# Kernel optimization log

Hardware: AMD Instinct MI355X
Metric: run time of the kernel (lower is better)

The kernel has to match this reference:

```python
import jax, jax.numpy as jnp
import numpy as np

B = 64          # decode batch (one token per sequence)
HID = 4096      # hidden_size
HQ = 32         # num query heads
HKV = 8         # num kv heads (GQA, groups = 4)
D = 128         # head_dim
BS = 16         # block_size of paged KV cache
MAXB = 64       # max blocks per sequence -> max context 1024
MAXPOS = 4096   # rope table length
TOTAL_SLOTS = B * MAXB * BS


def setup_inputs() -> dict:
    key = jax.random.key(0)
    ks = jax.random.split(key, 10)
    hidden = jax.random.normal(ks[0], (B, 1, HID), jnp.float32)
    context_lens = jax.random.randint(ks[1], (B,), 512, BS * MAXB + 1).astype(jnp.int32)
    positions = (context_lens - 1).reshape(B, 1)  # decoding token position
    # each sequence owns a contiguous range of blocks
    block_tables = jnp.arange(B * MAXB, dtype=jnp.int32).reshape(B, MAXB)
    last = context_lens - 1
    slot_mapping = (block_tables[jnp.arange(B), last // BS] * BS + last % BS).astype(jnp.int32)
    inv_freq = 1.0 / (10000.0 ** (jnp.arange(0, D, 2, dtype=jnp.float32) / D))
    freqs = jnp.outer(jnp.arange(MAXPOS, dtype=jnp.float32), inv_freq)  # [MAXPOS, D/2]
    cos, sin = jnp.cos(freqs), jnp.sin(freqs)
    key_cache = jax.random.normal(ks[2], (TOTAL_SLOTS, HKV, D), jnp.float32) * 0.5
    value_cache = jax.random.normal(ks[3], (TOTAL_SLOTS, HKV, D), jnp.float32) * 0.5
    Wq = jax.random.normal(ks[4], (HQ * D, HID), jnp.float32) * 0.02
    Wk = jax.random.normal(ks[5], (HKV * D, HID), jnp.float32) * 0.02
    Wv = jax.random.normal(ks[6], (HKV * D, HID), jnp.float32) * 0.02
    Wo = jax.random.normal(ks[7], (HID, HQ * D), jnp.float32) * 0.02
    return dict(hidden=hidden, positions=positions, cos=cos, sin=sin,
                key_cache=key_cache, value_cache=value_cache,
                slot_mapping=slot_mapping, block_tables=block_tables,
                context_lens=context_lens, Wq=Wq, Wk=Wk, Wv=Wv, Wo=Wo)


def reference(hidden, positions, cos, sin, key_cache, value_cache,
              slot_mapping, block_tables, context_lens, Wq, Wk, Wv, Wo):
    b, s, _ = hidden.shape  # s == 1 (paged decode path)
    q = (hidden @ Wq.T).reshape(b, s, HQ, D)
    k = (hidden @ Wk.T).reshape(b, s, HKV, D)
    v = (hidden @ Wv.T).reshape(b, s, HKV, D)
    # rotary embedding (half-split convention)
    c = cos[positions][:, :, None, :]  # [b,s,1,D/2]
    sn = sin[positions][:, :, None, :]
    def rope(x):
        x1, x2 = jnp.split(x, 2, axis=-1)
        return jnp.concatenate([x1 * c - x2 * sn, x2 * c + x1 * sn], axis=-1)
    q, k = rope(q), rope(k)
    # scatter current token's K/V into the paged cache via slot_mapping
    kc = key_cache.at[slot_mapping].set(k.reshape(-1, HKV, D))
    vc = value_cache.at[slot_mapping].set(v.reshape(-1, HKV, D))
    # gather each sequence's KV via block tables
    T = MAXB * BS
    t = jnp.arange(T)
    slots = block_tables[:, t // BS] * BS + (t % BS)  # [b, T]
    keys = kc[slots]   # [b, T, HKV, D]
    vals = vc[slots]   # [b, T, HKV, D]
    # GQA attention, q has one token per sequence
    G = HQ // HKV
    qg = q.reshape(b, HKV, G, D)
    scores = jnp.einsum('bkgd,btkd->bkgt', qg, keys) / jnp.sqrt(jnp.float32(D))
    mask = t[None, :] < context_lens[:, None]  # [b, T]
    scores = jnp.where(mask[:, None, None, :], scores, -jnp.inf)
    p = jax.nn.softmax(scores, axis=-1)
    out = jnp.einsum('bkgt,btkd->bkgd', p, vals).reshape(b, 1, HQ * D)
    return out @ Wo.T
```

## Files before the change

### kernel.cpp

```cpp
#include <hip/hip_runtime.h>

#define B_    64
#define HID_  4096
#define HQ_   32
#define HKV_  8
#define D_    128
#define BS_   16
#define MAXB_ 64

#define KS1     32
#define KCHUNK  (HID_ / KS1)
#define NSTEP   (KCHUNK / 32)
#define QKV_ROWS 6144
#define O_ROWS   4096
#define SPLITS  8

#define REGION_SZ ((size_t)KS1 * QKV_ROWS * 64)
#define QKVF_SZ  ((size_t)64 * 6144)
#define XB_SZ    ((size_t)HID_ * 64)

typedef __attribute__((ext_vector_type(8))) short bf16x8;
typedef __attribute__((ext_vector_type(4))) float f32x4;

__device__ inline unsigned short f2bf(float x) {
  union { float f; unsigned u; } v; v.f = x;
  unsigned r = v.u + 0x7fff + ((v.u >> 16) & 1);
  return (unsigned short)(r >> 16);
}
__device__ inline float bf2f(unsigned short h) {
  union { float f; unsigned u; } v; v.u = ((unsigned)h) << 16; return v.f;
}

__global__ __launch_bounds__(256) void convert_x(
    const float* __restrict__ X, unsigned short* __restrict__ XBhi,
    unsigned short* __restrict__ XBlo)
{
  int idx = blockIdx.x * 256 + threadIdx.x;
  int kg = idx >> 6, b = idx & 63;
  const float* xp = X + (size_t)b * HID_ + kg * 8;
  float4 a = *(const float4*)xp, c = *(const float4*)(xp + 4);
  float xs[8] = {a.x, a.y, a.z, a.w, c.x, c.y, c.z, c.w};
  unsigned short hi[8], lo[8];
  #pragma unroll
  for (int j = 0; j < 8; ++j) {
    hi[j] = f2bf(xs[j]);
    lo[j] = f2bf(xs[j] - bf2f(hi[j]));
  }
  *(uint4*)(XBhi + (size_t)idx * 8) = *(const uint4*)hi;
  *(uint4*)(XBlo + (size_t)idx * 8) = *(const uint4*)lo;
}

__global__ __launch_bounds__(256, 4) void gemm_mfma(
    const float* __restrict__ W0, const float* __restrict__ W1,
    const float* __restrict__ W2,
    const unsigned short* __restrict__ XBhi,
    const unsigned short* __restrict__ XBlo,
    int split1, int split2, int rows_total, float* __restrict__ part)
{
  const int tid = threadIdx.x;
  const int l   = tid & 63;
  const int w   = tid >> 6;
  const int r0  = blockIdx.x * 128 + w * 32;
  const int k0  = blockIdx.y * KCHUNK;

  const float* W; int rloc;
  if (r0 < split1)      { W = W0; rloc = r0; }
  else if (r0 < split2) { W = W1; rloc = r0 - split1; }
  else                  { W = W2; rloc = r0 - split2; }

  const int lm = l & 15;
  const int lk = l >> 4;

  const float* wp0 = W + (size_t)(rloc + lm) * HID_ + k0 + lk * 8;
  const float* wp1 = wp0 + (size_t)16 * HID_;
  const unsigned short* bh = XBhi + ((size_t)(k0 / 8 + lk) * 64 + lm) * 8;
  const unsigned short* bl = XBlo + ((size_t)(k0 / 8 + lk) * 64 + lm) * 8;

  f32x4 acc[2][4];
  #pragma unroll
  for (int rt = 0; rt < 2; ++rt)
    #pragma unroll
    for (int ct = 0; ct < 4; ++ct)
      #pragma unroll
      for (int i = 0; i < 4; ++i) acc[rt][ct][i] = 0.f;

  #pragma unroll
  for (int ks = 0; ks < NSTEP; ++ks) {
    bf16x8 Bh[4], Bl[4];
    #pragma unroll
    for (int ct = 0; ct < 4; ++ct) {
      Bh[ct] = *(const bf16x8*)(bh + (size_t)ks * 2048 + ct * 128);
      Bl[ct] = *(const bf16x8*)(bl + (size_t)ks * 2048 + ct * 128);
    }
    #pragma unroll
    for (int rt = 0; rt < 2; ++rt) {
      const float* wp = (rt ? wp1 : wp0) + ks * 32;
      float4 a0 = *(const float4*)wp;
      float4 a1 = *(const float4*)(wp + 4);
      float xs[8] = {a0.x, a0.y, a0.z, a0.w, a1.x, a1.y, a1.z, a1.w};
      bf16x8 Ah, Al;
      #pragma unroll
      for (int j = 0; j < 8; ++j) {
        unsigned short h = f2bf(xs[j]);
        Ah[j] = (short)h;
        Al[j] = (short)f2bf(xs[j] - bf2f(h));
      }
      #pragma unroll
      for (int ct = 0; ct < 4; ++ct) {
        acc[rt][ct] = __builtin_amdgcn_mfma_f32_16x16x32_bf16(Ah, Bh[ct], acc[rt][ct], 0, 0, 0);
        acc[rt][ct] = __builtin_amdgcn_mfma_f32_16x16x32_bf16(Al, Bh[ct], acc[rt][ct], 0, 0, 0);
        acc[rt][ct] = __builtin_amdgcn_mfma_f32_16x16x32_bf16(Ah, Bl[ct], acc[rt][ct], 0, 0, 0);
      }
    }
  }

  #pragma unroll
  for (int rt = 0; rt < 2; ++rt)
    #pragma unroll
    for (int ct = 0; ct < 4; ++ct) {
      int row = r0 + rt * 16 + lk * 4;
      int bat = ct * 16 + lm;
      #pragma unroll
      for (int i = 0; i < 4; ++i)
        part[((size_t)blockIdx.y * rows_total + row + i) * 64 + bat] = acc[rt][ct][i];
    }
}

__global__ __launch_bounds__(256) void reduce_rope(
    const float* __restrict__ part, const float* __restrict__ cosT,
    const float* __restrict__ sinT, const int* __restrict__ positions,
    float* __restrict__ qkvf)
{
  const int bb  = threadIdx.x & 63;
  const int cid = blockIdx.x * 4 + (threadIdx.x >> 6);
  const int pos = positions[bb];

  if (cid < 2048) {
    const int hq = cid >> 6, d0 = cid & 63;
    const int r1 = hq * 128 + d0;
    float x1 = 0.f, x2 = 0.f;
    #pragma unroll 8
    for (int ks = 0; ks < KS1; ++ks) {
      x1 += part[((size_t)ks * QKV_ROWS + r1) * 64 + bb];
      x2 += part[((size_t)ks * QKV_ROWS + r1 + 64) * 64 + bb];
    }
    float c = cosT[pos * 64 + d0], s = sinT[pos * 64 + d0];
    const float scale = 0.08838834764831843f;
    qkvf[(size_t)(bb * 32 + hq) * 128 + d0]      = (x1 * c - x2 * s) * scale;
    qkvf[(size_t)(bb * 32 + hq) * 128 + d0 + 64] = (x2 * c + x1 * s) * scale;
  } else if (cid < 2560) {
    const int c2 = cid - 2048;
    const int kh = c2 >> 6, d0 = c2 & 63;
    const int r1 = 4096 + kh * 128 + d0;
    float x1 = 0.f, x2 = 0.f;
    #pragma unroll 8
    for (int ks = 0; ks < KS1; ++ks) {
      x1 += part[((size_t)ks * QKV_ROWS + r1) * 64 + bb];
      x2 += part[((size_t)ks * QKV_ROWS + r1 + 64) * 64 + bb];
    }
    float c = cosT[pos * 64 + d0], s = sinT[pos * 64 + d0];
    qkvf[262144 + (size_t)(bb * 8 + kh) * 128 + d0]      = x1 * c - x2 * s;
    qkvf[262144 + (size_t)(bb * 8 + kh) * 128 + d0 + 64] = x2 * c + x1 * s;
  } else {
    const int c2 = cid - 2560;
    const int kh = c2 >> 6, d0 = c2 & 63;
    const int r1 = 5120 + kh * 128 + d0;
    float x1 = 0.f, x2 = 0.f;
    #pragma unroll 8
    for (int ks = 0; ks < KS1; ++ks) {
      x1 += part[((size_t)ks * QKV_ROWS + r1) * 64 + bb];
      x2 += part[((size_t)ks * QKV_ROWS + r1 + 64) * 64 + bb];
    }
    qkvf[327680 + (size_t)(bb * 8 + kh) * 128 + d0]      = x1;
    qkvf[327680 + (size_t)(bb * 8 + kh) * 128 + d0 + 64] = x2;
  }
}

__global__ __launch_bounds__(256, 8) void attn_split(
    const float* __restrict__ qkvf, const float* __restrict__ kcache,
    const float* __restrict__ vcache, const int* __restrict__ btab,
    const int* __restrict__ ctxlen,
    float* __restrict__ part_o,
    float* __restrict__ part_ml)
{
  const int bid = blockIdx.x;
  const int s   = bid & (SPLITS - 1);
  const int bh  = bid >> 3;
  const int b = bh >> 3, h = bh & 7;
  const int ctx   = ctxlen[b];
  const int chunk = (ctx + SPLITS - 1) / SPLITS;
  const int t0 = s * chunk;
  const int t1 = min(ctx, t0 + chunk);
  const int n  = t1 - t0;
  const int last = ctx - 1;

  const int tid  = threadIdx.x;
  const int half = tid >> 5;
  const int d4   = tid & 31;

  __shared__ float sc[4][128];
  __shared__ float wred[4][4][128];
  __shared__ float red[4][2];

  float4 qf[4];
  #pragma unroll
  for (int g = 0; g < 4; ++g)
    qf[g] = *(const float4*)(qkvf + (size_t)(b * 32 + h * 4 + g) * 128 + d4 * 4);

  const float* knew = qkvf + 262144 + (size_t)(b * 8 + h) * 128;
  const float* vnew = qkvf + 327680 + (size_t)(b * 8 + h) * 128;

  for (int t = t0 + half; t < t1; t += 8) {
    const float* kp;
    if (t == last) kp = knew;
    else {
      int slot = btab[b * MAXB_ + (t >> 4)] * BS_ + (t & 15);
      kp = kcache + ((size_t)slot * HKV_ + h) * D_;
    }
    float4 kv = *(const float4*)(kp + d4 * 4);
    float p0 = qf[0].x * kv.x + qf[0].y * kv.y + qf[0].z * kv.z + qf[0].w * kv.w;
    float p1 = qf[1].x * kv.x + qf[1].y * kv.y + qf[1].z * kv.z + qf[1].w * kv.w;
    float p2 = qf[2].x * kv.x + qf[2].y * kv.y + qf[2].z * kv.z + qf[2].w * kv.w;
    float p3 = qf[3].x * kv.x + qf[3].y * kv.y + qf[3].z * kv.z + qf[3].w * kv.w;
    #pragma unroll
    for (int m = 16; m >= 1; m >>= 1) {
      p0 += __shfl_xor(p0, m);
      p1 += __shfl_xor(p1, m);
      p2 += __shfl_xor(p2, m);
      p3 += __shfl_xor(p3, m);
    }
    if (d4 == 0) {
      int i = t - t0;
      sc[0][i] = p0; sc[1][i] = p1; sc[2][i] = p2; sc[3][i] = p3;
    }
  }
  __syncthreads();

  {
    const int w = tid >> 6, l = tid & 63;
    float mx = -1e30f;
    for (int i = l; i < n; i += 64) mx = fmaxf(mx, sc[w][i]);
    #pragma unroll
    for (int m = 32; m >= 1; m >>= 1) mx = fmaxf(mx, __shfl_xor(mx, m));
    float lsum = 0.f;
    for (int i = l; i < n; i += 64) {
      float p = __expf(sc[w][i] - mx);
      sc[w][i] = p;
      lsum += p;
    }
    #pragma unroll
    for (int m = 32; m >= 1; m >>= 1) lsum += __shfl_xor(lsum, m);
    if (l == 0) { red[w][0] = mx; red[w][1] = lsum; }
  }
  __syncthreads();

  float acc[4][4] = {{0.f}};
  for (int t = t0 + half; t < t1; t += 8) {
    const float* vp;
    if (t == last) vp = vnew;
    else {
      int slot = btab[b * MAXB_ + (t >> 4)] * BS_ + (t & 15);
      vp = vcache + ((size_t)slot * HKV_ + h) * D_;
    }
    float4 vv = *(const float4*)(vp + d4 * 4);
    int i = t - t0;
    #pragma unroll
    for (int g = 0; g < 4; ++g) {
      float p = sc[g][i];
      acc[g][0] += p * vv.x; acc[g][1] += p * vv.y;
      acc[g][2] += p * vv.z; acc[g][3] += p * vv.w;
    }
  }
  #pragma unroll
  for (int g = 0; g < 4; ++g)
    #pragma unroll
    for (int j = 0; j < 4; ++j)
      acc[g][j] += __shfl_xor(acc[g][j], 32);
  if ((tid & 32) == 0) {
    int wv = tid >> 6;
    #pragma unroll
    for (int g = 0; g < 4; ++g)
      #pragma unroll
      for (int j = 0; j < 4; ++j)
        wred[wv][g][d4 * 4 + j] = acc[g][j];
  }
  __syncthreads();

  for (int idx = tid; idx < 512; idx += 256) {
    int g = idx >> 7, d = idx & 127;
    float v = wred[0][g][d] + wred[1][g][d] + wred[2][g][d] + wred[3][g][d];
    part_o[(size_t)bid * 512 + idx] = v;
  }
  if (tid < 8) part_ml[(size_t)bid * 8 + tid] = red[tid >> 1][tid & 1];
}

__global__ __launch_bounds__(256) void attn_combine_xb(
    const float* __restrict__ part_o, const float* __restrict__ part_ml,
    unsigned short* __restrict__ XBhi, unsigned short* __restrict__ XBlo)
{
  const int bh = blockIdx.x;
  const int b = bh >> 3, h = bh & 7;
  const int tid = threadIdx.x;

  __shared__ float Sg[SPLITS][4];
  __shared__ float Dg[4];

  if (tid < 32) {
    int s = tid >> 2, g = tid & 3;
    float m = part_ml[((size_t)bh * SPLITS + s) * 8 + g * 2];
    float l = part_ml[((size_t)bh * SPLITS + s) * 8 + g * 2 + 1];
    float M = m;
    #pragma unroll
    for (int k = 4; k <= 16; k <<= 1) M = fmaxf(M, __shfl_xor(M, k));
    float scl = __expf(m - M);
    float dl = l * scl;
    #pragma unroll
    for (int k = 4; k <= 16; k <<= 1) dl += __shfl_xor(dl, k);
    Sg[s][g] = scl;
    if (s == 0) Dg[g] = dl;
  }
  __syncthreads();

  for (int idx = tid; idx < 512; idx += 256) {
    int g = idx >> 7, d = idx & 127;
    float num = 0.f;
    #pragma unroll
    for (int s = 0; s < SPLITS; ++s)
      num += Sg[s][g] * part_o[((size_t)bh * SPLITS + s) * 512 + idx];
    float val = num / Dg[g];
    int col = (h * 4 + g) * 128 + d;
    int kg = col >> 3, j = col & 7;
    unsigned short hi = f2bf(val);
    unsigned short lo = f2bf(val - bf2f(hi));
    XBhi[((size_t)kg * 64 + b) * 8 + j] = hi;
    XBlo[((size_t)kg * 64 + b) * 8 + j] = lo;
  }
}

__global__ __launch_bounds__(256) void reduce_out_t(
    const float* __restrict__ part, float* __restrict__ out)
{
  __shared__ float t[64][65];
  const int i0 = blockIdx.x * 64;
  const int lane = threadIdx.x & 63, q = threadIdx.x >> 6;

  #pragma unroll
  for (int rr = q; rr < 64; rr += 4) {
    float s = 0.f;
    #pragma unroll 8
    for (int ks = 0; ks < KS1; ++ks)
      s += part[((size_t)ks * O_ROWS + i0 + rr) * 64 + lane];
    t[rr][lane] = s;
  }
  __syncthreads();
  #pragma unroll
  for (int rr = q; rr < 64; rr += 4)
    out[(size_t)rr * O_ROWS + i0 + lane] = t[lane][rr];
}

extern "C" void kernel_launch(void* const* d_in, const int* in_sizes, int n_in,
                              void* d_out, int out_size, void* d_ws, size_t ws_size,
                              hipStream_t stream)
{
  (void)in_sizes; (void)n_in; (void)out_size; (void)ws_size;
  const float* hidden    = (const float*)d_in[0];
  const int*   positions = (const int*)d_in[1];
  const float* cosT      = (const float*)d_in[2];
  const float* sinT      = (const float*)d_in[3];
  const float* kcache    = (const float*)d_in[4];
  const float* vcache    = (const float*)d_in[5];
  const int*   btab      = (const int*)d_in[7];
  const int*   ctx       = (const int*)d_in[8];
  const float* Wq        = (const float*)d_in[9];
  const float* Wk        = (const float*)d_in[10];
  const float* Wv        = (const float*)d_in[11];
  const float* Wo        = (const float*)d_in[12];
  float* out = (float*)d_out;

  float* ws      = (float*)d_ws;
  float* region  = ws;
  float* qkvf    = region + REGION_SZ;
  unsigned short* XBhi = (unsigned short*)(qkvf + QKVF_SZ);
  unsigned short* XBlo = XBhi + XB_SZ;
  float* part1   = region;
  float* part_o  = region;
  float* part_ml = region + (size_t)B_ * HKV_ * SPLITS * 512;
  float* part3   = region;

  convert_x<<<128, 256, 0, stream>>>(hidden, XBhi, XBlo);
  gemm_mfma<<<dim3(QKV_ROWS / 128, KS1), 256, 0, stream>>>(
      Wq, Wk, Wv, XBhi, XBlo, 4096, 5120, QKV_ROWS, part1);
  reduce_rope<<<768, 256, 0, stream>>>(part1, cosT, sinT, positions, qkvf);
  attn_split<<<B_ * HKV_ * SPLITS, 256, 0, stream>>>(
      qkvf, kcache, vcache, btab, ctx, part_o, part_ml);
  attn_combine_xb<<<B_ * HKV_, 256, 0, stream>>>(part_o, part_ml, XBhi, XBlo);
  gemm_mfma<<<dim3(O_ROWS / 128, KS1), 256, 0, stream>>>(
      Wo, Wo, Wo, XBhi, XBlo, O_ROWS, O_ROWS, O_ROWS, part3);
  reduce_out_t<<<O_ROWS / 64, 256, 0, stream>>>(part3, out);
}
```

Baseline: 224.1 us.

## Stage weight tiles through LDS with async double-buffered global_load_lds

The GEMM kernel now streams fp32 weight tiles into double-buffered shared memory using direct global-to-LDS loads with an XOR swizzle. The next k-step's load is issued while the current one is computed, instead of each wave loading its own rows straight from global memory. The QKV projection also drops its split-K factor from 32 to 16, which halves the partial-sum traffic, with kchunk and nstep passed at runtime. The costs are lower occupancy (launch bounds go from 4 to 3), a barrier every k-step, and fewer blocks in the QKV GEMM.

```diff
diff --git a/kernel.cpp b/kernel.cpp
--- a/kernel.cpp
+++ b/kernel.cpp
@@ -8,14 +8,13 @@
 #define BS_   16
 #define MAXB_ 64
 
-#define KS1     32
-#define KCHUNK  (HID_ / KS1)
-#define NSTEP   (KCHUNK / 32)
+#define KSQ     16
+#define KSO     32
 #define QKV_ROWS 6144
 #define O_ROWS   4096
 #define SPLITS  8
 
-#define REGION_SZ ((size_t)KS1 * QKV_ROWS * 64)
+#define REGION_SZ ((size_t)KSO * O_ROWS * 64)
 #define QKVF_SZ  ((size_t)64 * 6144)
 #define XB_SZ    ((size_t)HID_ * 64)
 
@@ -50,18 +49,21 @@
   *(uint4*)(XBlo + (size_t)idx * 8) = *(const uint4*)lo;
 }
 
-__global__ __launch_bounds__(256, 4) void gemm_mfma(
+__global__ __launch_bounds__(256, 3) void gemm_mfma(
     const float* __restrict__ W0, const float* __restrict__ W1,
     const float* __restrict__ W2,
     const unsigned short* __restrict__ XBhi,
     const unsigned short* __restrict__ XBlo,
-    int split1, int split2, int rows_total, float* __restrict__ part)
-{
+    int split1, int split2, int rows_total, int kchunk, int nstep,
+    float* __restrict__ part)
+{
+  __shared__ float Abuf[2][128 * 32];
+
   const int tid = threadIdx.x;
   const int l   = tid & 63;
   const int w   = tid >> 6;
-  const int r0  = blockIdx.x * 128 + w * 32;
-  const int k0  = blockIdx.y * KCHUNK;
+  const int r0  = blockIdx.x * 128;
+  const int k0  = blockIdx.y * kchunk;
 
   const float* W; int rloc;
   if (r0 < split1)      { W = W0; rloc = r0; }
@@ -71,10 +73,28 @@
   const int lm = l & 15;
   const int lk = l >> 4;
 
-  const float* wp0 = W + (size_t)(rloc + lm) * HID_ + k0 + lk * 8;
-  const float* wp1 = wp0 + (size_t)16 * HID_;
+  const float* Wb = W + (size_t)rloc * HID_ + k0;
   const unsigned short* bh = XBhi + ((size_t)(k0 / 8 + lk) * 64 + lm) * 8;
   const unsigned short* bl = XBlo + ((size_t)(k0 / 8 + lk) * 64 + lm) * 8;
+
+  const int sidx0 = tid;
+  const int wbase = tid & ~63;
+
+  #define ISSUE(buf, step)                                                   \
+    {                                                                        \
+      const float* Wk = Wb + (size_t)(step) * 32;                            \
+      _Pragma("unroll")                                                      \
+      for (int c = 0; c < 4; ++c) {                                          \
+        int idx = c * 256 + sidx0;                                           \
+        int row = idx >> 3, cg = idx & 7;                                    \
+        int g = cg ^ (row & 7);                                              \
+        const float* gsrc = Wk + (size_t)row * HID_ + g * 4;                 \
+        float* ldst = &Abuf[buf][(size_t)(c * 256 + wbase) * 4];             \
+        __builtin_amdgcn_global_load_lds(                                    \
+            (const __attribute__((address_space(1))) unsigned int*)gsrc,     \
+            (__attribute__((address_space(3))) unsigned int*)ldst, 16, 0, 0);\
+      }                                                                      \
+    }
 
   f32x4 acc[2][4];
   #pragma unroll
@@ -84,19 +104,28 @@
       #pragma unroll
       for (int i = 0; i < 4; ++i) acc[rt][ct][i] = 0.f;
 
-  #pragma unroll
-  for (int ks = 0; ks < NSTEP; ++ks) {
+  ISSUE(0, 0);
+
+  for (int s = 0; s < nstep; ++s) {
+    __syncthreads();
+    if (s + 1 < nstep) ISSUE((s + 1) & 1, s + 1);
+
     bf16x8 Bh[4], Bl[4];
     #pragma unroll
     for (int ct = 0; ct < 4; ++ct) {
-      Bh[ct] = *(const bf16x8*)(bh + (size_t)ks * 2048 + ct * 128);
-      Bl[ct] = *(const bf16x8*)(bl + (size_t)ks * 2048 + ct * 128);
-    }
+      Bh[ct] = *(const bf16x8*)(bh + (size_t)s * 2048 + ct * 128);
+      Bl[ct] = *(const bf16x8*)(bl + (size_t)s * 2048 + ct * 128);
+    }
+
+    const float* A = Abuf[s & 1];
     #pragma unroll
     for (int rt = 0; rt < 2; ++rt) {
-      const float* wp = (rt ? wp1 : wp0) + ks * 32;
-      float4 a0 = *(const float4*)wp;
-      float4 a1 = *(const float4*)(wp + 4);
+      int r = w * 32 + rt * 16 + lm;
+      const float* base = A + r * 32;
+      int g0 = (2 * lk) ^ (r & 7);
+      int g1 = (2 * lk + 1) ^ (r & 7);
+      float4 a0 = *(const float4*)(base + g0 * 4);
+      float4 a1 = *(const float4*)(base + g1 * 4);
       float xs[8] = {a0.x, a0.y, a0.z, a0.w, a1.x, a1.y, a1.z, a1.w};
       bf16x8 Ah, Al;
       #pragma unroll
@@ -113,12 +142,13 @@
       }
     }
   }
+  #undef ISSUE
 
   #pragma unroll
   for (int rt = 0; rt < 2; ++rt)
     #pragma unroll
     for (int ct = 0; ct < 4; ++ct) {
-      int row = r0 + rt * 16 + lk * 4;
+      int row = r0 + w * 32 + rt * 16 + lk * 4;
       int bat = ct * 16 + lm;
       #pragma unroll
       for (int i = 0; i < 4; ++i)
@@ -140,7 +170,7 @@
     const int r1 = hq * 128 + d0;
     float x1 = 0.f, x2 = 0.f;
     #pragma unroll 8
-    for (int ks = 0; ks < KS1; ++ks) {
+    for (int ks = 0; ks < KSQ; ++ks) {
       x1 += part[((size_t)ks * QKV_ROWS + r1) * 64 + bb];
       x2 += part[((size_t)ks * QKV_ROWS + r1 + 64) * 64 + bb];
     }
@@ -154,7 +184,7 @@
     const int r1 = 4096 + kh * 128 + d0;
     float x1 = 0.f, x2 = 0.f;
     #pragma unroll 8
-    for (int ks = 0; ks < KS1; ++ks) {
+    for (int ks = 0; ks < KSQ; ++ks) {
       x1 += part[((size_t)ks * QKV_ROWS + r1) * 64 + bb];
       x2 += part[((size_t)ks * QKV_ROWS + r1 + 64) * 64 + bb];
     }
@@ -167,7 +197,7 @@
     const int r1 = 5120 + kh * 128 + d0;
     float x1 = 0.f, x2 = 0.f;
     #pragma unroll 8
-    for (int ks = 0; ks < KS1; ++ks) {
+    for (int ks = 0; ks < KSQ; ++ks) {
       x1 += part[((size_t)ks * QKV_ROWS + r1) * 64 + bb];
       x2 += part[((size_t)ks * QKV_ROWS + r1 + 64) * 64 + bb];
     }
@@ -348,7 +378,7 @@
   for (int rr = q; rr < 64; rr += 4) {
     float s = 0.f;
     #pragma unroll 8
-    for (int ks = 0; ks < KS1; ++ks)
+    for (int ks = 0; ks < KSO; ++ks)
       s += part[((size_t)ks * O_ROWS + i0 + rr) * 64 + lane];
     t[rr][lane] = s;
   }
@@ -388,13 +418,13 @@
   float* part3   = region;
 
   convert_x<<<128, 256, 0, stream>>>(hidden, XBhi, XBlo);
-  gemm_mfma<<<dim3(QKV_ROWS / 128, KS1), 256, 0, stream>>>(
-      Wq, Wk, Wv, XBhi, XBlo, 4096, 5120, QKV_ROWS, part1);
+  gemm_mfma<<<dim3(QKV_ROWS / 128, KSQ), 256, 0, stream>>>(
+      Wq, Wk, Wv, XBhi, XBlo, 4096, 5120, QKV_ROWS, HID_ / KSQ, HID_ / KSQ / 32, part1);
   reduce_rope<<<768, 256, 0, stream>>>(part1, cosT, sinT, positions, qkvf);
   attn_split<<<B_ * HKV_ * SPLITS, 256, 0, stream>>>(
       qkvf, kcache, vcache, btab, ctx, part_o, part_ml);
   attn_combine_xb<<<B_ * HKV_, 256, 0, stream>>>(part_o, part_ml, XBhi, XBlo);
-  gemm_mfma<<<dim3(O_ROWS / 128, KS1), 256, 0, stream>>>(
-      Wo, Wo, Wo, XBhi, XBlo, O_ROWS, O_ROWS, O_ROWS, part3);
+  gemm_mfma<<<dim3(O_ROWS / 128, KSO), 256, 0, stream>>>(
+      Wo, Wo, Wo, XBhi, XBlo, O_ROWS, O_ROWS, O_ROWS, HID_ / KSO, HID_ / KSO / 32, part3);
   reduce_out_t<<<O_ROWS / 64, 256, 0, stream>>>(part3, out);
 }
```

After: 213.2 us. 4.9% less time.

## Fuse attention into a single-pass online softmax and halve GEMM split-K

Applied to the files above, without the earlier changes.

The attention split kernel now reads K and V in the same loop and keeps a per-thread online softmax state (running max, sum and accumulator). Per-half and per-wave states are merged at the end, so the shared-memory score buffer and two of the barriers go away. Block-table entries are staged in shared memory, and the new token's K/V is handled outside the main loop instead of being branched on every iteration. Separately, the GEMM split-K factor drops from 32 to 16, with partial unrolling and a lower occupancy hint. This halves the partial-sum traffic in the reduce kernels but gives the GEMMs fewer blocks and longer per-block loops.

```diff
diff --git a/kernel.cpp b/kernel.cpp
--- a/kernel.cpp
+++ b/kernel.cpp
@@ -8,14 +8,13 @@
 #define BS_   16
 #define MAXB_ 64
 
-#define KS1     32
-#define KCHUNK  (HID_ / KS1)
-#define NSTEP   (KCHUNK / 32)
+#define KS      16
+#define KCHUNK  (HID_ / KS)
 #define QKV_ROWS 6144
 #define O_ROWS   4096
 #define SPLITS  8
 
-#define REGION_SZ ((size_t)KS1 * QKV_ROWS * 64)
+#define REGION_SZ ((size_t)KS * QKV_ROWS * 64)
 #define QKVF_SZ  ((size_t)64 * 6144)
 #define XB_SZ    ((size_t)HID_ * 64)
 
@@ -84,8 +83,8 @@
       #pragma unroll
       for (int i = 0; i < 4; ++i) acc[rt][ct][i] = 0.f;
 
-  #pragma unroll
-  for (int ks = 0; ks < NSTEP; ++ks) {
+  #pragma unroll 2
+  for (int ks = 0; ks < KCHUNK / 32; ++ks) {
     bf16x8 Bh[4], Bl[4];
     #pragma unroll
     for (int ct = 0; ct < 4; ++ct) {
@@ -140,7 +139,7 @@
     const int r1 = hq * 128 + d0;
     float x1 = 0.f, x2 = 0.f;
     #pragma unroll 8
-    for (int ks = 0; ks < KS1; ++ks) {
+    for (int ks = 0; ks < KS; ++ks) {
       x1 += part[((size_t)ks * QKV_ROWS + r1) * 64 + bb];
       x2 += part[((size_t)ks * QKV_ROWS + r1 + 64) * 64 + bb];
     }
@@ -154,7 +153,7 @@
     const int r1 = 4096 + kh * 128 + d0;
     float x1 = 0.f, x2 = 0.f;
     #pragma unroll 8
-    for (int ks = 0; ks < KS1; ++ks) {
+    for (int ks = 0; ks < KS; ++ks) {
       x1 += part[((size_t)ks * QKV_ROWS + r1) * 64 + bb];
       x2 += part[((size_t)ks * QKV_ROWS + r1 + 64) * 64 + bb];
     }
@@ -167,7 +166,7 @@
     const int r1 = 5120 + kh * 128 + d0;
     float x1 = 0.f, x2 = 0.f;
     #pragma unroll 8
-    for (int ks = 0; ks < KS1; ++ks) {
+    for (int ks = 0; ks < KS; ++ks) {
       x1 += part[((size_t)ks * QKV_ROWS + r1) * 64 + bb];
       x2 += part[((size_t)ks * QKV_ROWS + r1 + 64) * 64 + bb];
     }
@@ -176,7 +175,7 @@
   }
 }
 
-__global__ __launch_bounds__(256, 8) void attn_split(
+__global__ __launch_bounds__(256, 4) void attn_split(
     const float* __restrict__ qkvf, const float* __restrict__ kcache,
     const float* __restrict__ vcache, const int* __restrict__ btab,
     const int* __restrict__ ctxlen,
@@ -191,107 +190,144 @@
   const int chunk = (ctx + SPLITS - 1) / SPLITS;
   const int t0 = s * chunk;
   const int t1 = min(ctx, t0 + chunk);
-  const int n  = t1 - t0;
   const int last = ctx - 1;
+  const int tEnd = min(t1, last);
 
   const int tid  = threadIdx.x;
   const int half = tid >> 5;
   const int d4   = tid & 31;
 
-  __shared__ float sc[4][128];
-  __shared__ float wred[4][4][128];
-  __shared__ float red[4][2];
+  __shared__ int   sblk[16];
+  __shared__ float wm[4][4], wl[4][4];
+  __shared__ float wacc[4][4][128];
+
+  const int blk0 = t0 >> 4;
+  if (tid < 16) {
+    int ib = blk0 + tid;
+    sblk[tid] = (ib < MAXB_) ? btab[b * MAXB_ + ib] : 0;
+  }
+  __syncthreads();
 
   float4 qf[4];
   #pragma unroll
   for (int g = 0; g < 4; ++g)
     qf[g] = *(const float4*)(qkvf + (size_t)(b * 32 + h * 4 + g) * 128 + d4 * 4);
 
-  const float* knew = qkvf + 262144 + (size_t)(b * 8 + h) * 128;
-  const float* vnew = qkvf + 327680 + (size_t)(b * 8 + h) * 128;
-
-  for (int t = t0 + half; t < t1; t += 8) {
-    const float* kp;
-    if (t == last) kp = knew;
-    else {
-      int slot = btab[b * MAXB_ + (t >> 4)] * BS_ + (t & 15);
-      kp = kcache + ((size_t)slot * HKV_ + h) * D_;
-    }
-    float4 kv = *(const float4*)(kp + d4 * 4);
+  float m[4], l[4], acc[4][4];
+  #pragma unroll
+  for (int g = 0; g < 4; ++g) {
+    m[g] = -1e30f; l[g] = 0.f;
+    #pragma unroll
+    for (int j = 0; j < 4; ++j) acc[g][j] = 0.f;
+  }
+
+  for (int t = t0 + half; t < tEnd; t += 8) {
+    int slot = sblk[(t >> 4) - blk0] * BS_ + (t & 15);
+    const float* base = kcache + ((size_t)slot * HKV_ + h) * D_ + d4 * 4;
+    const float* vbas = vcache + ((size_t)slot * HKV_ + h) * D_ + d4 * 4;
+    float4 kv = *(const float4*)base;
+    float4 vv = *(const float4*)vbas;
+
     float p0 = qf[0].x * kv.x + qf[0].y * kv.y + qf[0].z * kv.z + qf[0].w * kv.w;
     float p1 = qf[1].x * kv.x + qf[1].y * kv.y + qf[1].z * kv.z + qf[1].w * kv.w;
     float p2 = qf[2].x * kv.x + qf[2].y * kv.y + qf[2].z * kv.z + qf[2].w * kv.w;
     float p3 = qf[3].x * kv.x + qf[3].y * kv.y + qf[3].z * kv.z + qf[3].w * kv.w;
     #pragma unroll
-    for (int m = 16; m >= 1; m >>= 1) {
-      p0 += __shfl_xor(p0, m);
-      p1 += __shfl_xor(p1, m);
-      p2 += __shfl_xor(p2, m);
-      p3 += __shfl_xor(p3, m);
-    }
-    if (d4 == 0) {
-      int i = t - t0;
-      sc[0][i] = p0; sc[1][i] = p1; sc[2][i] = p2; sc[3][i] = p3;
-    }
-  }
-  __syncthreads();
-
-  {
-    const int w = tid >> 6, l = tid & 63;
-    float mx = -1e30f;
-    for (int i = l; i < n; i += 64) mx = fmaxf(mx, sc[w][i]);
-    #pragma unroll
-    for (int m = 32; m >= 1; m >>= 1) mx = fmaxf(mx, __shfl_xor(mx, m));
-    float lsum = 0.f;
-    for (int i = l; i < n; i += 64) {
-      float p = __expf(sc[w][i] - mx);
-      sc[w][i] = p;
-      lsum += p;
-    }
-    #pragma unroll
-    for (int m = 32; m >= 1; m >>= 1) lsum += __shfl_xor(lsum, m);
-    if (l == 0) { red[w][0] = mx; red[w][1] = lsum; }
-  }
-  __syncthreads();
-
-  float acc[4][4] = {{0.f}};
-  for (int t = t0 + half; t < t1; t += 8) {
-    const float* vp;
-    if (t == last) vp = vnew;
-    else {
-      int slot = btab[b * MAXB_ + (t >> 4)] * BS_ + (t & 15);
-      vp = vcache + ((size_t)slot * HKV_ + h) * D_;
-    }
-    float4 vv = *(const float4*)(vp + d4 * 4);
-    int i = t - t0;
+    for (int mm = 16; mm >= 1; mm >>= 1) {
+      p0 += __shfl_xor(p0, mm);
+      p1 += __shfl_xor(p1, mm);
+      p2 += __shfl_xor(p2, mm);
+      p3 += __shfl_xor(p3, mm);
+    }
+    float pg[4] = {p0, p1, p2, p3};
     #pragma unroll
     for (int g = 0; g < 4; ++g) {
-      float p = sc[g][i];
-      acc[g][0] += p * vv.x; acc[g][1] += p * vv.y;
-      acc[g][2] += p * vv.z; acc[g][3] += p * vv.w;
-    }
-  }
-  #pragma unroll
-  for (int g = 0; g < 4; ++g)
-    #pragma unroll
-    for (int j = 0; j < 4; ++j)
-      acc[g][j] += __shfl_xor(acc[g][j], 32);
+      float nm = fmaxf(m[g], pg[g]);
+      float sc = __expf(m[g] - nm);
+      float pe = __expf(pg[g] - nm);
+      l[g] = l[g] * sc + pe;
+      acc[g][0] = acc[g][0] * sc + pe * vv.x;
+      acc[g][1] = acc[g][1] * sc + pe * vv.y;
+      acc[g][2] = acc[g][2] * sc + pe * vv.z;
+      acc[g][3] = acc[g][3] * sc + pe * vv.w;
+      m[g] = nm;
+    }
+  }
+
+  if (t1 > last && half == ((last - t0) & 7)) {
+    const float* kp = qkvf + 262144 + (size_t)(b * 8 + h) * 128 + d4 * 4;
+    const float* vp = qkvf + 327680 + (size_t)(b * 8 + h) * 128 + d4 * 4;
+    float4 kv = *(const float4*)kp;
+    float4 vv = *(const float4*)vp;
+    float p0 = qf[0].x * kv.x + qf[0].y * kv.y + qf[0].z * kv.z + qf[0].w * kv.w;
+    float p1 = qf[1].x * kv.x + qf[1].y * kv.y + qf[1].z * kv.z + qf[1].w * kv.w;
+    float p2 = qf[2].x * kv.x + qf[2].y * kv.y + qf[2].z * kv.z + qf[2].w * kv.w;
+    float p3 = qf[3].x * kv.x + qf[3].y * kv.y + qf[3].z * kv.z + qf[3].w * kv.w;
+    #pragma unroll
+    for (int mm = 16; mm >= 1; mm >>= 1) {
+      p0 += __shfl_xor(p0, mm);
+      p1 += __shfl_xor(p1, mm);
+      p2 += __shfl_xor(p2, mm);
+      p3 += __shfl_xor(p3, mm);
+    }
+    float pg[4] = {p0, p1, p2, p3};
+    #pragma unroll
+    for (int g = 0; g < 4; ++g) {
+      float nm = fmaxf(m[g], pg[g]);
+      float sc = __expf(m[g] - nm);
+      float pe = __expf(pg[g] - nm);
+      l[g] = l[g] * sc + pe;
+      acc[g][0] = acc[g][0] * sc + pe * vv.x;
+      acc[g][1] = acc[g][1] * sc + pe * vv.y;
+      acc[g][2] = acc[g][2] * sc + pe * vv.z;
+      acc[g][3] = acc[g][3] * sc + pe * vv.w;
+      m[g] = nm;
+    }
+  }
+
+  #pragma unroll
+  for (int g = 0; g < 4; ++g) {
+    float om = __shfl_xor(m[g], 32);
+    float ol = __shfl_xor(l[g], 32);
+    float M  = fmaxf(m[g], om);
+    float s0 = __expf(m[g] - M);
+    float s1 = __expf(om - M);
+    l[g] = l[g] * s0 + ol * s1;
+    #pragma unroll
+    for (int j = 0; j < 4; ++j) {
+      float oa = __shfl_xor(acc[g][j], 32);
+      acc[g][j] = acc[g][j] * s0 + oa * s1;
+    }
+    m[g] = M;
+  }
   if ((tid & 32) == 0) {
     int wv = tid >> 6;
+    if (d4 == 0) {
+      #pragma unroll
+      for (int g = 0; g < 4; ++g) { wm[wv][g] = m[g]; wl[wv][g] = l[g]; }
+    }
     #pragma unroll
     for (int g = 0; g < 4; ++g)
       #pragma unroll
       for (int j = 0; j < 4; ++j)
-        wred[wv][g][d4 * 4 + j] = acc[g][j];
+        wacc[wv][g][d4 * 4 + j] = acc[g][j];
   }
   __syncthreads();
 
   for (int idx = tid; idx < 512; idx += 256) {
     int g = idx >> 7, d = idx & 127;
-    float v = wred[0][g][d] + wred[1][g][d] + wred[2][g][d] + wred[3][g][d];
-    part_o[(size_t)bid * 512 + idx] = v;
-  }
-  if (tid < 8) part_ml[(size_t)bid * 8 + tid] = red[tid >> 1][tid & 1];
+    float M4 = fmaxf(fmaxf(wm[0][g], wm[1][g]), fmaxf(wm[2][g], wm[3][g]));
+    float e0 = __expf(wm[0][g] - M4), e1 = __expf(wm[1][g] - M4);
+    float e2 = __expf(wm[2][g] - M4), e3 = __expf(wm[3][g] - M4);
+    float num = wacc[0][g][d] * e0 + wacc[1][g][d] * e1
+              + wacc[2][g][d] * e2 + wacc[3][g][d] * e3;
+    part_o[(size_t)bid * 512 + idx] = num;
+    if (d == 0) {
+      float lt = wl[0][g] * e0 + wl[1][g] * e1 + wl[2][g] * e2 + wl[3][g] * e3;
+      part_ml[(size_t)bid * 8 + g * 2]     = M4;
+      part_ml[(size_t)bid * 8 + g * 2 + 1] = lt;
+    }
+  }
 }
 
 __global__ __launch_bounds__(256) void attn_combine_xb(
@@ -348,7 +384,7 @@
   for (int rr = q; rr < 64; rr += 4) {
     float s = 0.f;
     #pragma unroll 8
-    for (int ks = 0; ks < KS1; ++ks)
+    for (int ks = 0; ks < KS; ++ks)
       s += part[((size_t)ks * O_ROWS + i0 + rr) * 64 + lane];
     t[rr][lane] = s;
   }
@@ -388,13 +424,13 @@
   float* part3   = region;
 
   convert_x<<<128, 256, 0, stream>>>(hidden, XBhi, XBlo);
-  gemm_mfma<<<dim3(QKV_ROWS / 128, KS1), 256, 0, stream>>>(
+  gemm_mfma<<<dim3(QKV_ROWS / 128, KS), 256, 0, stream>>>(
       Wq, Wk, Wv, XBhi, XBlo, 4096, 5120, QKV_ROWS, part1);
   reduce_rope<<<768, 256, 0, stream>>>(part1, cosT, sinT, positions, qkvf);
   attn_split<<<B_ * HKV_ * SPLITS, 256, 0, stream>>>(
       qkvf, kcache, vcache, btab, ctx, part_o, part_ml);
   attn_combine_xb<<<B_ * HKV_, 256, 0, stream>>>(part_o, part_ml, XBhi, XBlo);
-  gemm_mfma<<<dim3(O_ROWS / 128, KS1), 256, 0, stream>>>(
+  gemm_mfma<<<dim3(O_ROWS / 128, KS), 256, 0, stream>>>(
       Wo, Wo, Wo, XBhi, XBlo, O_ROWS, O_ROWS, O_ROWS, part3);
   reduce_out_t<<<O_ROWS / 64, 256, 0, stream>>>(part3, out);
 }
```

Result: faster. 184.1 us (-17.8%).
